# Kernel optimization log

Measured on AMD Instinct MI355X. Metric: run time of the kernel, lower is better.

## Reference

```python
import jax, jax.numpy as jnp
import numpy as np

T, N, E, F_IN, H_GNN, H_OUT, RH, G, C = 8, 10000, 160000, 128, 128, 128, 128, 32, 10


def gcn_layer(x, src, dst, W, b):
    # PyG GCNConv: h = D^-1/2 (A+I) D^-1/2 (x W) + b, self-loops added, edge weight 1
    h = x @ W  # [N, H]
    ones = jnp.ones((E,), h.dtype)
    deg = jax.ops.segment_sum(ones, dst, num_segments=N) + 1.0  # +1 for self-loop
    dinv = jax.lax.rsqrt(deg)
    coef = dinv[src] * dinv[dst]  # [E]
    agg = jax.ops.segment_sum(h[src] * coef[:, None], dst, num_segments=N)
    agg = agg + h * (dinv * dinv)[:, None]  # self-loop term
    return agg + b


def snapshot_encode(x, edge_index, batch, W1, b1, W2, b2):
    src, dst = edge_index[0], edge_index[1]
    h = jax.nn.relu(gcn_layer(x, src, dst, W1, b1))
    h = jax.nn.relu(gcn_layer(h, src, dst, W2, b2))
    sums = jax.ops.segment_sum(h, batch, num_segments=G)  # global_mean_pool
    cnts = jax.ops.segment_sum(jnp.ones((N,), h.dtype), batch, num_segments=G)
    return sums / jnp.maximum(cnts, 1.0)[:, None]  # [G, H_OUT]


def gru_layer(seq, Wih, Whh, bih, bhh):
    # seq: [T, G, in]; torch nn.GRU cell equations
    H = Whh.shape[1]

    def step(h, xt):
        gi = xt @ Wih.T + bih
        gh = h @ Whh.T + bhh
        ir, iz, inn = jnp.split(gi, 3, axis=-1)
        hr, hz, hn = jnp.split(gh, 3, axis=-1)
        r = jax.nn.sigmoid(ir + hr)
        z = jax.nn.sigmoid(iz + hz)
        n = jnp.tanh(inn + r * hn)
        h_new = (1.0 - z) * n + z * h
        return h_new, h_new

    h0 = jnp.zeros((seq.shape[1], H), seq.dtype)
    hT, outs = jax.lax.scan(step, h0, seq)
    return outs, hT


def setup_inputs() -> dict:
    key = jax.random.key(0)
    ks = jax.random.split(key, 20)
    s = 0.05
    inp = {
        "x": jax.random.normal(ks[0], (T, N, F_IN), jnp.float32),
        "edge_index": jax.random.randint(ks[1], (T, 2, E), 0, N),
        "batch": jax.random.randint(ks[2], (T, N), 0, G),
        "W1": jax.random.normal(ks[3], (F_IN, H_GNN), jnp.float32) * s,
        "b1": jnp.zeros((H_GNN,), jnp.float32),
        "W2": jax.random.normal(ks[4], (H_GNN, H_OUT), jnp.float32) * s,
        "b2": jnp.zeros((H_OUT,), jnp.float32),
        "Wih0": jax.random.normal(ks[5], (3 * RH, H_OUT), jnp.float32) * s,
        "Whh0": jax.random.normal(ks[6], (3 * RH, RH), jnp.float32) * s,
        "bih0": jnp.zeros((3 * RH,), jnp.float32),
        "bhh0": jnp.zeros((3 * RH,), jnp.float32),
        "Wih1": jax.random.normal(ks[7], (3 * RH, RH), jnp.float32) * s,
        "Whh1": jax.random.normal(ks[8], (3 * RH, RH), jnp.float32) * s,
        "bih1": jnp.zeros((3 * RH,), jnp.float32),
        "bhh1": jnp.zeros((3 * RH,), jnp.float32),
        "Wc": jax.random.normal(ks[9], (C, RH), jnp.float32) * s,
        "bc": jnp.zeros((C,), jnp.float32),
    }
    return inp


def reference(x, edge_index, batch, W1, b1, W2, b2, Wih0, Whh0, bih0, bhh0,
              Wih1, Whh1, bih1, bhh1, Wc, bc):
    # per-snapshot GNN encode, vmapped over T snapshots -> [T, G, H_OUT]
    emb = jax.vmap(snapshot_encode, in_axes=(0, 0, 0, None, None, None, None))(
        x, edge_index, batch, W1, b1, W2, b2)
    outs, _ = gru_layer(emb, Wih0, Whh0, bih0, bhh0)
    _, hT = gru_layer(outs, Wih1, Whh1, bih1, bhh1)  # h_n[-1]: last layer final state
    return hT @ Wc.T + bc  # [G, C]
```

## Files before the change

kernel.cpp:

```cpp
#include <hip/hip_runtime.h>

#define T_ 8
#define N_ 10000
#define E_ 160000
#define G_ 32
#define C_ 10
#define F_ 128

typedef _Float16 f16;
typedef _Float16 f16x2 __attribute__((ext_vector_type(2)));
typedef _Float16 f16x4 __attribute__((ext_vector_type(4)));
typedef _Float16 f16x8 __attribute__((ext_vector_type(8)));
typedef float floatx4 __attribute__((ext_vector_type(4)));

static constexpr int NSL = 16;
static constexpr int SLICE = E_ / NSL;

static constexpr size_t OFF_H2    = 0;
static constexpr size_t OFF_G     = 20480000;
static constexpr size_t OFF_H1    = 40960000;
static constexpr size_t OFF_REC   = 61440000;
static constexpr size_t OFF_CNT   = 66560000;
static constexpr size_t OFF_DINV  = 71680000;
static constexpr size_t OFF_RP    = 72000000;
static constexpr size_t OFF_CNTG  = 72320032;
static constexpr size_t OFF_BRP   = 72321056;
static constexpr size_t OFF_WP    = 72322112;
static constexpr size_t OFF_BLIST = 72387648;
static constexpr size_t OFF_GPACK = 72707648;
static constexpr size_t OFF_PART  = 73100864;

__device__ __forceinline__ float sig_fast(float x) {
  return __builtin_amdgcn_rcpf(1.0f + __builtin_amdgcn_exp2f(-1.4426950408889634f * x));
}
__device__ __forceinline__ float tanh_fast(float x) {
  return 1.0f - 2.0f * __builtin_amdgcn_rcpf(1.0f + __builtin_amdgcn_exp2f(2.8853900817779268f * x));
}

__global__ __launch_bounds__(1024) void prep0_kernel(const int* __restrict__ ei,
                                                     const int* __restrict__ batch,
                                                     int* __restrict__ cnt,
                                                     int* __restrict__ cntG,
                                                     const float* __restrict__ W1,
                                                     const float* __restrict__ W2,
                                                     f16* __restrict__ Wp,
                                                     const float* __restrict__ A0,
                                                     const float* __restrict__ A1,
                                                     const float* __restrict__ A2,
                                                     const float* __restrict__ A3,
                                                     f16* __restrict__ gp) {
  __shared__ int hL[N_];
  __shared__ int cL[G_];
  int b = blockIdx.x, tid = threadIdx.x;
  if (b >= 128) {
    int idx = (b - 128) * 1024 + tid;
    if (idx < 32768) {
      const float* W = (idx < 16384) ? W1 : W2;
      int l = idx & 16383;
      int j = l & 7, lane = (l >> 3) & 63, ct = (l >> 9) & 7, kc = (l >> 12) & 3;
      int k = kc * 32 + ((lane >> 4) & 3) * 8 + j;
      int n = ct * 16 + (lane & 15);
      Wp[idx] = (f16)W[k * 128 + n];
    } else {
      int gidx = idx - 32768;
      int mat = gidx / 49152, l = gidx - mat * 49152;
      int j = l & 7, lane = (l >> 3) & 63, kc = (l >> 9) & 3, nt = l >> 11;
      int k = kc * 32 + ((lane >> 4) & 3) * 8 + j;
      int u = nt * 16 + (lane & 15);
      const float* W = (mat == 0) ? A0 : (mat == 1) ? A1 : (mat == 2) ? A2 : A3;
      gp[gidx] = (f16)W[u * 128 + k];
    }
    return;
  }
  int t = b & 7, s = b >> 3;
  for (int i = tid; i < N_; i += 1024) hL[i] = 0;
  if (tid < G_) cL[tid] = 0;
  __syncthreads();
  const int* dstp = ei + (size_t)t * 2 * E_ + E_ + s * SLICE;
  for (int e4 = tid; e4 < SLICE / 4; e4 += 1024) {
    int4 d = *(const int4*)(dstp + e4 * 4);
    atomicAdd(&hL[d.x], 1); atomicAdd(&hL[d.y], 1);
    atomicAdd(&hL[d.z], 1); atomicAdd(&hL[d.w], 1);
  }
  if (s == 0)
    for (int n = tid; n < N_; n += 1024) atomicAdd(&cL[batch[t * N_ + n]], 1);
  __syncthreads();
  int* cp = cnt + ((size_t)t * NSL + s) * N_;
  for (int i = tid; i < N_; i += 1024) cp[i] = hL[i];
  if (s == 0 && tid < G_) cntG[t * G_ + tid] = cL[tid];
}

__global__ __launch_bounds__(1024) void scan_kernel(int* __restrict__ cnt,
                                                    int* __restrict__ rp,
                                                    float* __restrict__ dinv,
                                                    const int* __restrict__ cntG,
                                                    int* __restrict__ brp) {
  __shared__ int wsum[16];
  __shared__ int carry;
  int t = blockIdx.x, tid = threadIdx.x, lane = tid & 63, wid = tid >> 6;
  if (t == 8) {
    int v = (tid < 256) ? cntG[tid] : 0;
    for (int ofs = 1; ofs < 64; ofs <<= 1) {
      int u = __shfl_up(v, ofs);
      if (lane >= ofs) v += u;
    }
    if (lane == 63 && wid < 4) wsum[wid] = v;
    __syncthreads();
    if (tid < 256) {
      int base = 0;
      for (int w = 0; w < wid; ++w) base += wsum[w];
      if (tid == 0) brp[0] = 0;
      brp[tid + 1] = v + base;
    }
    return;
  }
  if (tid == 0) { carry = 0; rp[t * (N_ + 1)] = 0; }
  __syncthreads();
  for (int c0 = 0; c0 < N_; c0 += 1024) {
    int n = c0 + tid;
    int vs[NSL];
    int deg = 0;
    if (n < N_) {
#pragma unroll
      for (int s = 0; s < NSL; ++s) {
        vs[s] = cnt[((size_t)t * NSL + s) * N_ + n];
        deg += vs[s];
      }
      dinv[t * N_ + n] = rsqrtf((float)deg + 1.0f);
    }
    int v = (n < N_) ? deg : 0;
    int v0 = v;
    for (int ofs = 1; ofs < 64; ofs <<= 1) {
      int u = __shfl_up(v, ofs);
      if (lane >= ofs) v += u;
    }
    if (lane == 63) wsum[wid] = v;
    __syncthreads();
    if (wid == 0) {
      int w = (lane < 16) ? wsum[lane] : 0;
      for (int ofs = 1; ofs < 16; ofs <<= 1) {
        int u = __shfl_up(w, ofs);
        if (lane >= ofs) w += u;
      }
      if (lane < 16) wsum[lane] = w;
    }
    __syncthreads();
    int base = carry + (wid ? wsum[wid - 1] : 0);
    if (n < N_) {
      rp[t * (N_ + 1) + n + 1] = base + v;
      int run = base + v - v0;
#pragma unroll
      for (int s = 0; s < NSL; ++s) {
        int vv = vs[s];
        cnt[((size_t)t * NSL + s) * N_ + n] = run;
        run += vv;
      }
    }
    __syncthreads();
    if (tid == 0) carry += wsum[15];
    __syncthreads();
  }
}

__global__ __launch_bounds__(1024) void gxfill_kernel(const float* __restrict__ x,
                                                      const f16* __restrict__ Wp,
                                                      f16* __restrict__ Gout,
                                                      const float* __restrict__ dinv,
                                                      const int* __restrict__ ei,
                                                      const int* __restrict__ base,
                                                      int* __restrict__ rec,
                                                      const int* __restrict__ batch,
                                                      const int* __restrict__ brp,
                                                      int* __restrict__ blist) {
  __shared__ union {
    f16x8 Bp[2048];
    struct { int offL[N_]; int cb[G_]; } fl;
  } U;
  int b = blockIdx.x, tid = threadIdx.x;
  if (b < 313) {
    const f16x8* Wv = (const f16x8*)Wp;
    for (int i = tid; i < 2048; i += 1024) U.Bp[i] = Wv[i];
    __syncthreads();
    int stid = tid & 255;
    int sub = tid >> 8;
    int wave = stid >> 6, lane = stid & 63;
    int quad = lane >> 4, m = lane & 15;
    int rowbase = b * 256 + sub * 64 + wave * 16;
    if (rowbase >= 80000) return;
    floatx4 acc[8];
#pragma unroll
    for (int ct = 0; ct < 8; ++ct) { floatx4 z = {0.f, 0.f, 0.f, 0.f}; acc[ct] = z; }
#pragma unroll
    for (int kc = 0; kc < 4; ++kc) {
      const float* Ar = x + (size_t)(rowbase + m) * F_ + kc * 32 + quad * 8;
      float4 lo = *(const float4*)Ar;
      float4 hi = *(const float4*)(Ar + 4);
      f16x8 a;
      a[0] = (f16)lo.x; a[1] = (f16)lo.y; a[2] = (f16)lo.z; a[3] = (f16)lo.w;
      a[4] = (f16)hi.x; a[5] = (f16)hi.y; a[6] = (f16)hi.z; a[7] = (f16)hi.w;
#pragma unroll
      for (int ct = 0; ct < 8; ++ct)
        acc[ct] = __builtin_amdgcn_mfma_f32_16x16x32_f16(a, U.Bp[(kc * 8 + ct) * 64 + lane],
                                                         acc[ct], 0, 0, 0);
    }
    float sv[4];
#pragma unroll
    for (int r = 0; r < 4; ++r) sv[r] = dinv[rowbase + quad * 4 + r];
#pragma unroll
    for (int ct = 0; ct < 8; ++ct) {
      int colc = ct * 16 + m;
#pragma unroll
      for (int r = 0; r < 4; ++r)
        Gout[(size_t)(rowbase + quad * 4 + r) * F_ + colc] = (f16)(acc[ct][r] * sv[r]);
    }
    return;
  }
  int b2 = b - 313;
  int t = b2 & 7, s = b2 >> 3;
  const int* bp = base + ((size_t)t * NSL + s) * N_;
  for (int i = tid; i < N_; i += 1024) U.fl.offL[i] = bp[i];
  if (s == 0 && tid < G_) U.fl.cb[tid] = brp[t * G_ + tid];
  __syncthreads();
  const int* srcp = ei + (size_t)t * 2 * E_ + s * SLICE;
  const int* dstp = srcp + E_;
  int* rt = rec + (size_t)t * E_;
  for (int e4 = tid; e4 < SLICE / 4; e4 += 1024) {
    int4 sv = *(const int4*)(srcp + e4 * 4);
    int4 dv = *(const int4*)(dstp + e4 * 4);
    int p0 = atomicAdd(&U.fl.offL[dv.x], 1);
    int p1 = atomicAdd(&U.fl.offL[dv.y], 1);
    int p2 = atomicAdd(&U.fl.offL[dv.z], 1);
    int p3 = atomicAdd(&U.fl.offL[dv.w], 1);
    rt[p0] = sv.x; rt[p1] = sv.y; rt[p2] = sv.z; rt[p3] = sv.w;
  }
  if (s == 0) {
    for (int n = tid; n < N_; n += 1024) {
      int g = batch[t * N_ + n];
      int p = atomicAdd(&U.fl.cb[g], 1);
      blist[p] = t * N_ + n;
    }
  }
}

__global__ __launch_bounds__(256) void gemm_kernel(const f16* __restrict__ A,
                                                   const f16* __restrict__ Wp,
                                                   f16* __restrict__ O) {
  __shared__ f16x8 Bp[2048];
  const f16x8* Wv = (const f16x8*)Wp;
  for (int i = threadIdx.x; i < 2048; i += 256) Bp[i] = Wv[i];
  __syncthreads();
  int wave = threadIdx.x >> 6, lane = threadIdx.x & 63;
  int quad = lane >> 4, m = lane & 15;
  int rowbase = blockIdx.x * 64 + wave * 16;
  const f16x8* Arow = (const f16x8*)(A + (size_t)(rowbase + m) * F_);
  floatx4 acc[8];
#pragma unroll
  for (int ct = 0; ct < 8; ++ct) { floatx4 z = {0.f, 0.f, 0.f, 0.f}; acc[ct] = z; }
#pragma unroll
  for (int kc = 0; kc < 4; ++kc) {
    f16x8 a = Arow[kc * 4 + quad];
#pragma unroll
    for (int ct = 0; ct < 8; ++ct)
      acc[ct] = __builtin_amdgcn_mfma_f32_16x16x32_f16(a, Bp[(kc * 8 + ct) * 64 + lane],
                                                       acc[ct], 0, 0, 0);
  }
#pragma unroll
  for (int ct = 0; ct < 8; ++ct) {
    int colc = ct * 16 + m;
#pragma unroll
    for (int r = 0; r < 4; ++r)
      O[(size_t)(rowbase + quad * 4 + r) * F_ + colc] = (f16)acc[ct][r];
  }
}

template <int SCALE_OUT>
__global__ __launch_bounds__(256) void agg_kernel(const f16* __restrict__ X, f16* __restrict__ O,
                                                  const int* __restrict__ rp,
                                                  const int* __restrict__ rec,
                                                  const float* __restrict__ dinv,
                                                  const float* __restrict__ bias) {
  int wave = threadIdx.x >> 6, lane = threadIdx.x & 63;
  int eg = lane >> 4;
  int cb = (lane & 15) * 8;
  int b = blockIdx.x;
  int t = b & 7, i = b >> 3;
  int n = i * 4 + wave;
  int row = t * N_ + n;
  float ds = dinv[row];
  int beg = rp[t * (N_ + 1) + n], end = rp[t * (N_ + 1) + n + 1];
  beg = __builtin_amdgcn_readfirstlane(beg);
  end = __builtin_amdgcn_readfirstlane(end);
  const int* rcb = rec + (size_t)t * E_ + beg + eg;
  const f16* Xt = X + (size_t)t * N_ * F_;

  float s[8] = {0.f, 0.f, 0.f, 0.f, 0.f, 0.f, 0.f, 0.f};
  if (eg == 3) {
    f16x8 v = *(const f16x8*)(Xt + (size_t)n * F_ + cb);
#pragma unroll
    for (int j = 0; j < 8; ++j) s[j] += (float)v[j];
  }
  int cnt = end - beg;
  int nq = cnt >> 2;
  if (nq > 0) {
    int rid0 = rcb[0];
    int rid1 = (nq > 1) ? rcb[4] : 0;
    int rid2 = (nq > 2) ? rcb[8] : 0;
    f16x8 vA = *(const f16x8*)(Xt + (size_t)rid0 * F_ + cb);
    f16x8 vB, vC;
    if (nq > 1) vB = *(const f16x8*)(Xt + (size_t)rid1 * F_ + cb);
    if (nq > 2) vC = *(const f16x8*)(Xt + (size_t)rid2 * F_ + cb);
    int ridN = (nq > 3) ? rcb[12] : 0;
    for (int q = 0; q + 3 < nq; ++q) {
      f16x8 vD = *(const f16x8*)(Xt + (size_t)ridN * F_ + cb);
      int ridNN = rcb[(q + 4) * 4];
#pragma unroll
      for (int j = 0; j < 8; ++j) s[j] += (float)vA[j];
      vA = vB; vB = vC; vC = vD; ridN = ridNN;
    }
#pragma unroll
    for (int j = 0; j < 8; ++j) s[j] += (float)vA[j];
    if (nq > 1) {
#pragma unroll
      for (int j = 0; j < 8; ++j) s[j] += (float)vB[j];
    }
    if (nq > 2) {
#pragma unroll
      for (int j = 0; j < 8; ++j) s[j] += (float)vC[j];
    }
  }
  int rem = cnt & 3;
  if (eg < rem) {
    int rid = rcb[nq * 4];
    f16x8 v = *(const f16x8*)(Xt + (size_t)rid * F_ + cb);
#pragma unroll
    for (int j = 0; j < 8; ++j) s[j] += (float)v[j];
  }
#pragma unroll
  for (int j = 0; j < 8; ++j) {
    s[j] += __shfl_xor(s[j], 16);
    s[j] += __shfl_xor(s[j], 32);
  }
  if (eg == 0) {
    float4 b0 = *(const float4*)(bias + cb);
    float4 b1v = *(const float4*)(bias + cb + 4);
    float bb[8] = {b0.x, b0.y, b0.z, b0.w, b1v.x, b1v.y, b1v.z, b1v.w};
    f16x8 o;
#pragma unroll
    for (int j = 0; j < 8; ++j) {
      float v = fmaxf(ds * s[j] + bb[j], 0.0f);
      if (SCALE_OUT) v *= ds;
      o[j] = (f16)v;
    }
    *(f16x8*)(O + (size_t)row * F_ + cb) = o;
  }
}

__global__ void pool1_kernel(const f16* __restrict__ H, const int* __restrict__ brp,
                             const int* __restrict__ blist, float* __restrict__ part) {
  int b = blockIdx.x;
  int wave = threadIdx.x >> 6, lane = threadIdx.x & 63;
  int idx = b >> 1;
  int s = (b & 1) * 4 + wave;
  int beg = brp[idx], end = brp[idx + 1];
  beg = __builtin_amdgcn_readfirstlane(beg);
  end = __builtin_amdgcn_readfirstlane(end);
  int len = end - beg;
  int lo = beg + (int)(((long long)len * s) >> 3);
  int hi = beg + (int)(((long long)len * (s + 1)) >> 3);
  float a00 = 0.f, a01 = 0.f, a10 = 0.f, a11 = 0.f;
  float a20 = 0.f, a21 = 0.f, a30 = 0.f, a31 = 0.f;
  int e = lo;
  for (; e + 3 < hi; e += 4) {
    int r0 = blist[e], r1 = blist[e + 1], r2 = blist[e + 2], r3 = blist[e + 3];
    f16x2 v0 = *(const f16x2*)(H + (size_t)r0 * F_ + 2 * lane);
    f16x2 v1 = *(const f16x2*)(H + (size_t)r1 * F_ + 2 * lane);
    f16x2 v2 = *(const f16x2*)(H + (size_t)r2 * F_ + 2 * lane);
    f16x2 v3 = *(const f16x2*)(H + (size_t)r3 * F_ + 2 * lane);
    a00 += (float)v0.x; a01 += (float)v0.y;
    a10 += (float)v1.x; a11 += (float)v1.y;
    a20 += (float)v2.x; a21 += (float)v2.y;
    a30 += (float)v3.x; a31 += (float)v3.y;
  }
  for (; e < hi; ++e) {
    int r = blist[e];
    f16x2 v = *(const f16x2*)(H + (size_t)r * F_ + 2 * lane);
    a00 += (float)v.x; a01 += (float)v.y;
  }
  float2 o;
  o.x = (a00 + a10) + (a20 + a30);
  o.y = (a01 + a11) + (a21 + a31);
  *(float2*)(part + ((size_t)idx * 8 + s) * F_ + 2 * lane) = o;
}

__global__ __launch_bounds__(256, 1) void gru_mega(
    const f16* __restrict__ gp, const float* __restrict__ part,
    const int* __restrict__ brp,
    const float* __restrict__ bih0, const float* __restrict__ bhh0,
    const float* __restrict__ bih1, const float* __restrict__ bhh1,
    const float* __restrict__ Wc, const float* __restrict__ bc,
    float* __restrict__ out) {
  __shared__ f16 emb_l[16][136];
  __shared__ float gib0[16][384];
  __shared__ f16 hb0[16 * 136];
  __shared__ f16 hb1[16 * 136];
  __shared__ float ghb[2 * 384];
  __shared__ float gib[2 * 384];
  __shared__ float h1s[2 * 128];
  int tid = threadIdx.x, wave = tid >> 6, lane = tid & 63;
  int quad = lane >> 4, mm = lane & 15;
  int g2 = tid >> 7, f = tid & 127;
  int bid = blockIdx.x;

  {
    int r = tid >> 4;
    int fb = (tid & 15) * 8;
    int idx = (r >> 1) * G_ + bid * 2 + (r & 1);
    float s[8] = {0.f, 0.f, 0.f, 0.f, 0.f, 0.f, 0.f, 0.f};
#pragma unroll
    for (int k = 0; k < 8; ++k) {
      const float* p = part + ((size_t)idx * 8 + k) * F_ + fb;
      float4 v0 = *(const float4*)p;
      float4 v1 = *(const float4*)(p + 4);
      s[0] += v0.x; s[1] += v0.y; s[2] += v0.z; s[3] += v0.w;
      s[4] += v1.x; s[5] += v1.y; s[6] += v1.z; s[7] += v1.w;
    }
    float d = fmaxf((float)(brp[idx + 1] - brp[idx]), 1.0f);
    f16x8 ev;
#pragma unroll
    for (int j = 0; j < 8; ++j) ev[j] = (f16)(s[j] / d);
    *(f16x8*)(&emb_l[r][fb]) = ev;
  }
  __syncthreads();

  {
    floatx4 acc[6];
#pragma unroll
    for (int i = 0; i < 6; ++i) { floatx4 z = {0.f, 0.f, 0.f, 0.f}; acc[i] = z; }
#pragma unroll
    for (int kc = 0; kc < 4; ++kc) {
      f16x8 a = *(const f16x8*)(&emb_l[mm][kc * 32 + quad * 8]);
#pragma unroll
      for (int i = 0; i < 6; ++i) {
        int nt = wave * 6 + i;
        f16x8 bf = *(const f16x8*)(gp + (size_t)((nt * 4 + kc) * 64 + lane) * 8);
        acc[i] = __builtin_amdgcn_mfma_f32_16x16x32_f16(a, bf, acc[i], 0, 0, 0);
      }
    }
#pragma unroll
    for (int i = 0; i < 6; ++i)
#pragma unroll
      for (int r = 0; r < 4; ++r)
        gib0[quad * 4 + r][(wave * 6 + i) * 16 + mm] = acc[i][r];
  }

  f16x8 B0[24], B1[24];
#pragma unroll
  for (int i = 0; i < 6; ++i)
#pragma unroll
    for (int kc = 0; kc < 4; ++kc) {
      size_t off = (size_t)((((wave * 6 + i) * 4 + kc) * 64 + lane)) * 8;
      B0[i * 4 + kc] = *(const f16x8*)(gp + 1 * 49152 + off);
      B1[i * 4 + kc] = *(const f16x8*)(gp + 3 * 49152 + off);
    }
  float br0 = bih0[f] + bhh0[f];
  float bz0 = bih0[128 + f] + bhh0[128 + f];
  float bni0 = bih0[256 + f], bnh0 = bhh0[256 + f];
  float br1 = bih1[f] + bhh1[f];
  float bz1 = bih1[128 + f] + bhh1[128 + f];
  float bni1 = bih1[256 + f], bnh1 = bhh1[256 + f];

  for (int i = tid; i < 16 * 136; i += 256) { hb0[i] = (f16)0.f; hb1[i] = (f16)0.f; }
  float h0 = 0.f, h1 = 0.f;
  __syncthreads();

  const f16* wih1 = gp + 2 * 49152;
  for (int t = 0; t < T_; ++t) {
    f16x8 Bs[24];
#pragma unroll
    for (int i = 0; i < 6; ++i)
#pragma unroll
      for (int kc = 0; kc < 4; ++kc)
        Bs[i * 4 + kc] = *(const f16x8*)(wih1 +
            (size_t)((((wave * 6 + i) * 4 + kc) * 64 + lane)) * 8);
    const float* gi = &gib0[t * 2 + g2][0];
    float gir = gi[f], giz = gi[128 + f], gin = gi[256 + f];

    floatx4 acc[6];
#pragma unroll
    for (int i = 0; i < 6; ++i) { floatx4 z = {0.f, 0.f, 0.f, 0.f}; acc[i] = z; }
#pragma unroll
    for (int kc = 0; kc < 4; ++kc) {
      f16x8 a = *(const f16x8*)(hb0 + mm * 136 + kc * 32 + quad * 8);
#pragma unroll
      for (int i = 0; i < 6; ++i)
        acc[i] = __builtin_amdgcn_mfma_f32_16x16x32_f16(a, B0[i * 4 + kc], acc[i], 0, 0, 0);
    }
    if (quad == 0) {
#pragma unroll
      for (int i = 0; i < 6; ++i) {
        ghb[0 * 384 + wave * 96 + i * 16 + mm] = acc[i][0];
        ghb[1 * 384 + wave * 96 + i * 16 + mm] = acc[i][1];
      }
    }
    __syncthreads();

    {
      float hr = ghb[g2 * 384 + f];
      float hz = ghb[g2 * 384 + 128 + f];
      float hn = ghb[g2 * 384 + 256 + f];
      float r = sig_fast(gir + hr + br0);
      float z = sig_fast(giz + hz + bz0);
      float nn = tanh_fast(gin + bni0 + r * (hn + bnh0));
      h0 = (1.0f - z) * nn + z * h0;
      hb0[g2 * 136 + f] = (f16)h0;
    }
    __syncthreads();

    floatx4 accx[6], acch[6];
#pragma unroll
    for (int i = 0; i < 6; ++i) {
      floatx4 z = {0.f, 0.f, 0.f, 0.f}; accx[i] = z; acch[i] = z;
    }
#pragma unroll
    for (int kc = 0; kc < 4; ++kc) {
      f16x8 ax = *(const f16x8*)(hb0 + mm * 136 + kc * 32 + quad * 8);
      f16x8 ah = *(const f16x8*)(hb1 + mm * 136 + kc * 32 + quad * 8);
#pragma unroll
      for (int i = 0; i < 6; ++i) {
        accx[i] = __builtin_amdgcn_mfma_f32_16x16x32_f16(ax, Bs[i * 4 + kc], accx[i], 0, 0, 0);
        acch[i] = __builtin_amdgcn_mfma_f32_16x16x32_f16(ah, B1[i * 4 + kc], acch[i], 0, 0, 0);
      }
    }
    if (quad == 0) {
#pragma unroll
      for (int i = 0; i < 6; ++i) {
        gib[0 * 384 + wave * 96 + i * 16 + mm] = accx[i][0];
        gib[1 * 384 + wave * 96 + i * 16 + mm] = accx[i][1];
        ghb[0 * 384 + wave * 96 + i * 16 + mm] = acch[i][0];
        ghb[1 * 384 + wave * 96 + i * 16 + mm] = acch[i][1];
      }
    }
    __syncthreads();

    {
      float i1r = gib[g2 * 384 + f];
      float i1z = gib[g2 * 384 + 128 + f];
      float i1n = gib[g2 * 384 + 256 + f];
      float hr = ghb[g2 * 384 + f];
      float hz = ghb[g2 * 384 + 128 + f];
      float hn = ghb[g2 * 384 + 256 + f];
      float r = sig_fast(i1r + hr + br1);
      float z = sig_fast(i1z + hz + bz1);
      float nn = tanh_fast(i1n + bni1 + r * (hn + bnh1));
      h1 = (1.0f - z) * nn + z * h1;
      hb1[g2 * 136 + f] = (f16)h1;
    }
    __syncthreads();
  }

  h1s[g2 * 128 + f] = h1;
  __syncthreads();
  if (tid < 2 * C_) {
    int gg = tid / C_, c = tid - gg * C_;
    float s = bc[c];
    const float* wr = Wc + (size_t)c * 128;
    const float* hr = h1s + gg * 128;
    for (int k = 0; k < 128; k += 4) {
      float4 w = *(const float4*)(wr + k);
      s += hr[k] * w.x + hr[k + 1] * w.y + hr[k + 2] * w.z + hr[k + 3] * w.w;
    }
    out[(bid * 2 + gg) * C_ + c] = s;
  }
}

extern "C" void kernel_launch(void* const* d_in, const int* in_sizes, int n_in,
                              void* d_out, int out_size, void* d_ws, size_t ws_size,
                              hipStream_t stream) {
  const float* x    = (const float*)d_in[0];
  const int*   ei   = (const int*)d_in[1];
  const int*   batch= (const int*)d_in[2];
  const float* W1   = (const float*)d_in[3];
  const float* b1   = (const float*)d_in[4];
  const float* W2   = (const float*)d_in[5];
  const float* b2   = (const float*)d_in[6];
  const float* Wih0 = (const float*)d_in[7];
  const float* Whh0 = (const float*)d_in[8];
  const float* bih0 = (const float*)d_in[9];
  const float* bhh0 = (const float*)d_in[10];
  const float* Wih1 = (const float*)d_in[11];
  const float* Whh1 = (const float*)d_in[12];
  const float* bih1 = (const float*)d_in[13];
  const float* bhh1 = (const float*)d_in[14];
  const float* Wc   = (const float*)d_in[15];
  const float* bc   = (const float*)d_in[16];
  float* out = (float*)d_out;

  char* ws = (char*)d_ws;
  f16*   H2    = (f16*)(ws + OFF_H2);
  f16*   G     = (f16*)(ws + OFF_G);
  f16*   H1p   = (f16*)(ws + OFF_H1);
  int*   rec   = (int*)(ws + OFF_REC);
  int*   cnt   = (int*)(ws + OFF_CNT);
  float* dinv  = (float*)(ws + OFF_DINV);
  int*   rp    = (int*)(ws + OFF_RP);
  int*   cntG  = (int*)(ws + OFF_CNTG);
  int*   brp   = (int*)(ws + OFF_BRP);
  f16*   Wp    = (f16*)(ws + OFF_WP);
  int*   blist = (int*)(ws + OFF_BLIST);
  f16*   gp    = (f16*)(ws + OFF_GPACK);
  float* part  = (float*)(ws + OFF_PART);

  prep0_kernel<<<352, 1024, 0, stream>>>(ei, batch, cnt, cntG,
                                         W1, W2, Wp, Wih0, Whh0, Wih1, Whh1, gp);
  scan_kernel<<<9, 1024, 0, stream>>>(cnt, rp, dinv, cntG, brp);
  gxfill_kernel<<<441, 1024, 0, stream>>>(x, Wp, G, dinv, ei, cnt, rec, batch, brp, blist);

  agg_kernel<1><<<20000, 256, 0, stream>>>(G, H1p, rp, rec, dinv, b1);
  gemm_kernel<<<1250, 256, 0, stream>>>(H1p, Wp + 16384, G);
  agg_kernel<0><<<20000, 256, 0, stream>>>(G, H2, rp, rec, dinv, b2);

  pool1_kernel<<<512, 256, 0, stream>>>(H2, brp, blist, part);
  gru_mega<<<16, 256, 0, stream>>>(gp, part, brp, bih0, bhh0, bih1, bhh1, Wc, bc, out);
}
```

Baseline: 288.7 us.

## Split degree scan into three kernels and hoist GRU Wih1 fragment loads

The single 9-block scan kernel, which serially read and rewrote the 16 per-slice counts for every node, is split into three kernels. An 80-block kernel sums the degrees and computes dinv, the 9-block kernel scans only the compact degree array, and a second 80-block kernel writes the per-slice offsets. This spreads the heavy count traffic across many CUs instead of leaving it on 8 blocks. In the GRU kernel, the Wih1 B-fragments are loaded into registers once, before the time loop, instead of every step. That adds register pressure and two extra kernel launches.

```diff
diff --git a/kernel.cpp b/kernel.cpp
--- a/kernel.cpp
+++ b/kernel.cpp
@@ -29,6 +29,7 @@
 static constexpr size_t OFF_BLIST = 72387648;
 static constexpr size_t OFF_GPACK = 72707648;
 static constexpr size_t OFF_PART  = 73100864;
+static constexpr size_t OFF_DEG   = 74149440;
 
 __device__ __forceinline__ float sig_fast(float x) {
   return __builtin_amdgcn_rcpf(1.0f + __builtin_amdgcn_exp2f(-1.4426950408889634f * x));
@@ -90,11 +91,24 @@
   if (s == 0 && tid < G_) cntG[t * G_ + tid] = cL[tid];
 }
 
-__global__ __launch_bounds__(1024) void scan_kernel(int* __restrict__ cnt,
-                                                    int* __restrict__ rp,
-                                                    float* __restrict__ dinv,
-                                                    const int* __restrict__ cntG,
-                                                    int* __restrict__ brp) {
+__global__ __launch_bounds__(1024) void scan1_kernel(const int* __restrict__ cnt,
+                                                     int* __restrict__ deg,
+                                                     float* __restrict__ dinv) {
+  int b = blockIdx.x, tid = threadIdx.x;
+  int t = b & 7, chunk = b >> 3;
+  int n = chunk * 1000 + tid;
+  if (tid >= 1000) return;
+  int d = 0;
+#pragma unroll
+  for (int s = 0; s < NSL; ++s) d += cnt[((size_t)t * NSL + s) * N_ + n];
+  deg[t * N_ + n] = d;
+  dinv[t * N_ + n] = rsqrtf((float)d + 1.0f);
+}
+
+__global__ __launch_bounds__(1024) void scan2_kernel(const int* __restrict__ deg,
+                                                     int* __restrict__ rp,
+                                                     const int* __restrict__ cntG,
+                                                     int* __restrict__ brp) {
   __shared__ int wsum[16];
   __shared__ int carry;
   int t = blockIdx.x, tid = threadIdx.x, lane = tid & 63, wid = tid >> 6;
@@ -118,18 +132,7 @@
   __syncthreads();
   for (int c0 = 0; c0 < N_; c0 += 1024) {
     int n = c0 + tid;
-    int vs[NSL];
-    int deg = 0;
-    if (n < N_) {
-#pragma unroll
-      for (int s = 0; s < NSL; ++s) {
-        vs[s] = cnt[((size_t)t * NSL + s) * N_ + n];
-        deg += vs[s];
-      }
-      dinv[t * N_ + n] = rsqrtf((float)deg + 1.0f);
-    }
-    int v = (n < N_) ? deg : 0;
-    int v0 = v;
+    int v = (n < N_) ? deg[t * N_ + n] : 0;
     for (int ofs = 1; ofs < 64; ofs <<= 1) {
       int u = __shfl_up(v, ofs);
       if (lane >= ofs) v += u;
@@ -146,19 +149,26 @@
     }
     __syncthreads();
     int base = carry + (wid ? wsum[wid - 1] : 0);
-    if (n < N_) {
-      rp[t * (N_ + 1) + n + 1] = base + v;
-      int run = base + v - v0;
-#pragma unroll
-      for (int s = 0; s < NSL; ++s) {
-        int vv = vs[s];
-        cnt[((size_t)t * NSL + s) * N_ + n] = run;
-        run += vv;
-      }
-    }
+    if (n < N_) rp[t * (N_ + 1) + n + 1] = base + v;
     __syncthreads();
     if (tid == 0) carry += wsum[15];
     __syncthreads();
+  }
+}
+
+__global__ __launch_bounds__(1024) void scan3_kernel(int* __restrict__ cnt,
+                                                     const int* __restrict__ rp) {
+  int b = blockIdx.x, tid = threadIdx.x;
+  int t = b & 7, chunk = b >> 3;
+  int n = chunk * 1000 + tid;
+  if (tid >= 1000) return;
+  int run = rp[t * (N_ + 1) + n];
+#pragma unroll
+  for (int s = 0; s < NSL; ++s) {
+    size_t idx = ((size_t)t * NSL + s) * N_ + n;
+    int v = cnt[idx];
+    cnt[idx] = run;
+    run += v;
   }
 }
 
@@ -453,7 +463,8 @@
         gib0[quad * 4 + r][(wave * 6 + i) * 16 + mm] = acc[i][r];
   }
 
-  f16x8 B0[24], B1[24];
+  f16x8 B0[24], B1[24], Bs[24];
+  const f16* wih1 = gp + 2 * 49152;
 #pragma unroll
   for (int i = 0; i < 6; ++i)
 #pragma unroll
@@ -461,6 +472,7 @@
       size_t off = (size_t)((((wave * 6 + i) * 4 + kc) * 64 + lane)) * 8;
       B0[i * 4 + kc] = *(const f16x8*)(gp + 1 * 49152 + off);
       B1[i * 4 + kc] = *(const f16x8*)(gp + 3 * 49152 + off);
+      Bs[i * 4 + kc] = *(const f16x8*)(wih1 + off);
     }
   float br0 = bih0[f] + bhh0[f];
   float bz0 = bih0[128 + f] + bhh0[128 + f];
@@ -473,15 +485,7 @@
   float h0 = 0.f, h1 = 0.f;
   __syncthreads();
 
-  const f16* wih1 = gp + 2 * 49152;
   for (int t = 0; t < T_; ++t) {
-    f16x8 Bs[24];
-#pragma unroll
-    for (int i = 0; i < 6; ++i)
-#pragma unroll
-      for (int kc = 0; kc < 4; ++kc)
-        Bs[i * 4 + kc] = *(const f16x8*)(wih1 +
-            (size_t)((((wave * 6 + i) * 4 + kc) * 64 + lane)) * 8);
     const float* gi = &gib0[t * 2 + g2][0];
     float gir = gi[f], giz = gi[128 + f], gin = gi[256 + f];
 
@@ -609,10 +613,13 @@
   int*   blist = (int*)(ws + OFF_BLIST);
   f16*   gp    = (f16*)(ws + OFF_GPACK);
   float* part  = (float*)(ws + OFF_PART);
+  int*   deg   = (int*)(ws + OFF_DEG);
 
   prep0_kernel<<<352, 1024, 0, stream>>>(ei, batch, cnt, cntG,
                                          W1, W2, Wp, Wih0, Whh0, Wih1, Whh1, gp);
-  scan_kernel<<<9, 1024, 0, stream>>>(cnt, rp, dinv, cntG, brp);
+  scan1_kernel<<<80, 1024, 0, stream>>>(cnt, deg, dinv);
+  scan2_kernel<<<9, 1024, 0, stream>>>(deg, rp, cntG, brp);
+  scan3_kernel<<<80, 1024, 0, stream>>>(cnt, rp);
   gxfill_kernel<<<441, 1024, 0, stream>>>(x, Wp, G, dinv, ei, cnt, rec, batch, brp, blist);
 
   agg_kernel<1><<<20000, 256, 0, stream>>>(G, H1p, rp, rec, dinv, b1);
```

After: 284.5 us. About the same (-1.5%).
